# Performance work log

Hardware: AMD Instinct MI355X
Metric: run time of the kernel (lower is better)

Reference implementation:

```python
import jax, jax.numpy as jnp
import numpy as np

BATCH, SEQ, D_MODEL = 2, 4096, 1024
D_STATE, EXPAND = 64, 2
D_INNER = D_MODEL * EXPAND


def setup_inputs() -> dict:
    key = jax.random.key(0)
    ks = jax.random.split(key, 12)
    s = 0.02
    return {
        "x": jax.random.normal(ks[0], (BATCH, SEQ, D_MODEL), dtype=jnp.float32),
        "W_in": jax.random.normal(ks[1], (D_MODEL, 2 * D_INNER), dtype=jnp.float32) * s,
        "b_in": jnp.zeros((2 * D_INNER,), dtype=jnp.float32),
        "W_xp": jax.random.normal(ks[2], (D_INNER, D_STATE), dtype=jnp.float32) * s,
        "b_xp": jnp.zeros((D_STATE,), dtype=jnp.float32),
        "W_dt": jax.random.normal(ks[3], (D_INNER, D_MODEL), dtype=jnp.float32) * s,
        "b_dt": jnp.zeros((D_MODEL,), dtype=jnp.float32),
        "W_out": jax.random.normal(ks[4], (D_INNER, D_MODEL), dtype=jnp.float32) * s,
        "b_out": jnp.zeros((D_MODEL,), dtype=jnp.float32),
        "A_log": jax.random.normal(ks[5], (D_STATE,), dtype=jnp.float32),
        "D": jax.random.normal(ks[6], (D_MODEL,), dtype=jnp.float32),
    }


def _silu(v):
    return v * jax.nn.sigmoid(v)


def reference(x, W_in, b_in, W_xp, b_xp, W_dt, b_dt, W_out, b_out, A_log, D):
    # in_proj -> split into inner stream and residual gate
    xr = x @ W_in + b_in                       # [B,S,2*d_inner]
    x_inner, res = jnp.split(xr, 2, axis=-1)   # each [B,S,d_inner]
    x_inner = _silu(x_inner)

    A = -jnp.exp(A_log)                        # [N]
    delta = jax.nn.softplus(x_inner @ W_dt + b_dt)  # [B,S,d_model]
    mean_delta = delta.mean(axis=-1)           # [B,S] (scalar dt per step, as in source)
    a = jnp.exp(A[None, None, :] * mean_delta[..., None])  # [B,S,N] discrete A
    bx = x_inner @ W_xp + b_xp                 # [B,S,N] input injection

    # sequential selective-scan recurrence: state = a_t * state + bx_t
    def step(state, inp):
        a_t, bx_t = inp                        # [B,N] each
        state = a_t * state + bx_t
        return state, state.sum(axis=-1)       # emit per-batch scalar

    init = jnp.zeros((x.shape[0], D_STATE), dtype=x.dtype)
    _, s_sum = jax.lax.scan(step, init, (a.transpose(1, 0, 2), bx.transpose(1, 0, 2)))
    s_sum = s_sum.T                            # [B,S]

    y = s_sum[..., None] * x_inner             # [B,S,d_inner]
    y = y * _silu(res)
    out = y @ W_out + b_out + x * D
    return out
```

## Files before the change

### kernel.cpp

```cpp
#include <hip/hip_runtime.h>

#define SEQ 4096
#define DMODEL 1024
#define DSTATE 64
#define DINNER 2048
#define MROWS 8192
#define NCAT 1152
#define NCHUNK 64
#define LCHUNK 64

typedef __attribute__((ext_vector_type(8))) __bf16 bf16x8;
typedef __attribute__((ext_vector_type(8))) short short8;
typedef __attribute__((ext_vector_type(4))) float floatx4;

__device__ inline float bf2f(short s) {
  union { unsigned u; float f; } c;
  c.u = ((unsigned)(unsigned short)s) << 16;
  return c.f;
}
__device__ inline short f2bf(float f) {
  union { float f; unsigned u; } c; c.f = f;
  unsigned r = 0x7fffu + ((c.u >> 16) & 1u);
  return (short)((c.u + r) >> 16);
}
__device__ inline float silu_f(float v) {
  return v * __builtin_amdgcn_rcpf(1.f + __expf(-v));
}
__device__ inline float softplus_f(float v) {
  return fmaxf(v, 0.f) + log1pf(__expf(-fabsf(v)));
}
__device__ inline void gld_lds16(const void* g, void* l) {
  __builtin_amdgcn_global_load_lds(
      (__attribute__((address_space(1))) void*)g,
      (__attribute__((address_space(3))) void*)l, 16, 0, 0);
}

__device__ inline size_t permOff(int r, int k, int K) {
  return (((size_t)(r >> 4) * (K >> 3) + (k >> 3)) << 7) + ((r & 15) << 3) + (k & 7);
}

#define PP0 4096
#define PP1 (PP0 + 4096)
#define PP2 (PP1 + 2048)
#define PP3 (PP2 + 128)
#define PP4 (PP3 + 2048)

__device__ void tile_transpose_perm(const float* __restrict__ in, short* __restrict__ out,
                                    int R, int C, int bx, int by, float (*tile)[33]) {
  const int tx = threadIdx.x & 31, ty = threadIdx.x >> 5;
  const int cb = bx * 32, rb = by * 32;
#pragma unroll
  for (int i = 0; i < 32; i += 8) {
    int r = rb + ty + i, c = cb + tx;
    tile[ty + i][tx] = (r < R && c < C) ? in[(size_t)r * C + c] : 0.f;
  }
  __syncthreads();
#pragma unroll
  for (int i = 0; i < 32; i += 8) {
    int orow = cb + ty + i, oc = rb + tx;
    if (orow < C && oc < R) out[permOff(orow, oc, R)] = f2bf(tile[tx][ty + i]);
  }
}

__global__ void prepass_kernel(const float* __restrict__ x, short* __restrict__ x_bf,
                               const float* __restrict__ W_in, short* __restrict__ Wt_in,
                               const float* __restrict__ W_dt, const float* __restrict__ W_xp,
                               short* __restrict__ Bcat,
                               const float* __restrict__ W_out, short* __restrict__ Wt_out) {
  __shared__ float tile[32][33];
  const int blk = blockIdx.x;
  if (blk < PP0) {
    int o = blk * 256 + threadIdx.x;
    int m = o & 15, rest = o >> 4;
    int c = rest & 127, p = rest >> 7;
    const float* src = x + ((size_t)(p * 16 + m)) * 1024 + c * 8;
    float4 v0 = ((const float4*)src)[0];
    float4 v1 = ((const float4*)src)[1];
    short8 ov;
    ov[0] = f2bf(v0.x); ov[1] = f2bf(v0.y); ov[2] = f2bf(v0.z); ov[3] = f2bf(v0.w);
    ov[4] = f2bf(v1.x); ov[5] = f2bf(v1.y); ov[6] = f2bf(v1.z); ov[7] = f2bf(v1.w);
    ((short8*)x_bf)[o] = ov;
  } else if (blk < PP1) {
    int t = blk - PP0;
    tile_transpose_perm(W_in, Wt_in, 1024, 4096, t & 127, t >> 7, tile);
  } else if (blk < PP2) {
    int t = blk - PP1;
    tile_transpose_perm(W_dt, Bcat, 2048, 1024, t & 31, t >> 5, tile);
  } else if (blk < PP3) {
    int t = blk - PP2;
    tile_transpose_perm(W_xp, Bcat + (size_t)1024 * DINNER, 2048, 64, t & 1, t >> 1, tile);
  } else {
    int t = blk - PP3;
    tile_transpose_perm(W_out, Wt_out, 2048, 1024, t & 31, t >> 5, tile);
  }
}

template <int MODE, int KTOT, int KSL, int NB, int Z>
__global__ __launch_bounds__(256) void gemm_bt(
    const short* __restrict__ A, const short* __restrict__ Bt,
    const float* __restrict__ bias,
    void* __restrict__ out0, void* __restrict__ out1)
{
  __shared__ __attribute__((aligned(16))) short sA[128 * 64];
  __shared__ __attribute__((aligned(16))) short sB[128 * 64];

  const int tid = threadIdx.x;
  const int lane = tid & 63;
  const int w = tid >> 6;
  const int wr = w >> 1, wc = w & 1;
  const int m = lane & 15, quad = lane >> 4;

  const int xcd = blockIdx.x & 7;
  const int rest = blockIdx.x >> 3;
  constexpr int PXB = 8 * NB;
  const int z = rest / PXB;
  const int q2 = rest - z * PXB;
  const int bM = (xcd * 8 + (q2 & 7)) * 128;
  const int bN = (q2 >> 3) * 128;
  constexpr int N = NB * 128;

  floatx4 acc[4][4] = {};

  const size_t PS = (size_t)KTOT * 16;
  const short* Apan0 = A  + ((size_t)(bM >> 4) + w) * PS + lane * 8;
  const short* Apan1 = Apan0 + 4 * PS;
  const short* Bpan0 = Bt + ((size_t)(bN >> 4) + w) * PS + lane * 8;
  const short* Bpan1 = Bpan0 + 4 * PS;
  short* dA0 = sA + w * 1024;
  short* dA1 = sA + (w + 4) * 1024;
  short* dB0 = sB + w * 1024;
  short* dB1 = sB + (w + 4) * 1024;

  const int kbeg = z * KSL;
  for (int k0 = kbeg; k0 < kbeg + KSL; k0 += 64) {
    __syncthreads();
    const size_t ko = (size_t)k0 * 16;
    gld_lds16(Apan0 + ko,       dA0);
    gld_lds16(Apan0 + ko + 512, dA0 + 512);
    gld_lds16(Apan1 + ko,       dA1);
    gld_lds16(Apan1 + ko + 512, dA1 + 512);
    gld_lds16(Bpan0 + ko,       dB0);
    gld_lds16(Bpan0 + ko + 512, dB0 + 512);
    gld_lds16(Bpan1 + ko,       dB1);
    gld_lds16(Bpan1 + ko + 512, dB1 + 512);
    __syncthreads();
#pragma unroll
    for (int kh = 0; kh < 2; ++kh) {
      bf16x8 af[4], bf[4];
#pragma unroll
      for (int rt = 0; rt < 4; ++rt)
        af[rt] = *(const bf16x8*)(sA + (wr * 4 + rt) * 1024 + (kh * 4 + quad) * 128 + m * 8);
#pragma unroll
      for (int ct = 0; ct < 4; ++ct)
        bf[ct] = *(const bf16x8*)(sB + (wc * 4 + ct) * 1024 + (kh * 4 + quad) * 128 + m * 8);
#pragma unroll
      for (int rt = 0; rt < 4; ++rt)
#pragma unroll
        for (int ct = 0; ct < 4; ++ct)
          acc[rt][ct] = __builtin_amdgcn_mfma_f32_16x16x32_bf16(af[rt], bf[ct], acc[rt][ct], 0, 0, 0);
    }
  }

  const int rowbase = bM + wr * 64;
  const int colbase = bN + wc * 64;

  if (MODE == 0) {
    short* dst = (bN < DINNER) ? (short*)out0 : (short*)out1;
    const int cb = (bN < DINNER) ? colbase : colbase - DINNER;
#pragma unroll
    for (int rt = 0; rt < 4; ++rt) {
      const size_t rowPan = ((size_t)((rowbase >> 4) + rt)) << 8;
#pragma unroll
      for (int ct = 0; ct < 4; ++ct) {
        const int colA = colbase + ct * 16 + m;
        const int colP = cb + ct * 16 + m;
        const size_t base = ((rowPan + (colP >> 3)) << 7) + (colP & 7) + ((size_t)quad * 32);
#pragma unroll
        for (int reg = 0; reg < 4; ++reg) {
          float val = acc[rt][ct][reg] + bias[colA];
          dst[base + reg * 8] = f2bf(silu_f(val));
        }
      }
    }
  } else {
    if (NB == 9 && colbase >= 1088) return;
    short* dst = (short*)out0 + (size_t)z * MROWS * N;
#pragma unroll
    for (int rt = 0; rt < 4; ++rt)
#pragma unroll
      for (int ct = 0; ct < 4; ++ct) {
        const int col = colbase + ct * 16 + m;
#pragma unroll
        for (int reg = 0; reg < 4; ++reg) {
          const int r = rowbase + rt * 16 + quad * 4 + reg;
          dst[(size_t)r * N + col] = f2bf(acc[rt][ct][reg]);
        }
      }
  }
}

template <int MODE, int KTOT, int KSL, int NT, int ZS>
__global__ __launch_bounds__(512, 2) void gemm256(
    const short* __restrict__ A, const short* __restrict__ Bt,
    const float* __restrict__ bias,
    void* __restrict__ out0, void* __restrict__ out1)
{
  __shared__ __attribute__((aligned(16))) short sA[4 * 8192];
  __shared__ __attribute__((aligned(16))) short sB[4 * 8192];

  const int tid = threadIdx.x;
  const int lane = tid & 63;
  const int w = tid >> 6;
  const int wr = w >> 2, wc = w & 3;
  const int m = lane & 15, quad = lane >> 4;

  const int xcd = blockIdx.x & 7;
  const int q = blockIdx.x >> 3;
  const int mt = xcd * 4 + (q & 3);
  const int rest = q >> 2;
  const int ntile = rest % NT;
  const int z = rest / NT;
  const int bM = mt * 256, bN = ntile * 256;
  const int kbeg = z * KSL;

  floatx4 acc[8][4] = {};

  const size_t PS = (size_t)KTOT * 16;
  const short* Ag0 = A  + ((size_t)(bM >> 4) + w) * PS + (size_t)kbeg * 16 + lane * 8;
  const short* Ag1 = Ag0 + 8 * PS;
  const short* Bg0 = Bt + ((size_t)(bN >> 4) + w) * PS + (size_t)kbeg * 16 + lane * 8;
  const short* Bg1 = Bg0 + 8 * PS;

  constexpr int NTILES = KSL / 32;

  auto STAGE = [&](int t, int slot) {
    const size_t go = (size_t)t << 9;
    short* da = sA + slot * 8192 + w * 512;
    short* db = sB + slot * 8192 + w * 512;
    gld_lds16(Ag0 + go, da);
    gld_lds16(Ag1 + go, da + 4096);
    gld_lds16(Bg0 + go, db);
    gld_lds16(Bg1 + go, db + 4096);
  };
  auto COMPUTE = [&](int slot) {
    const short* sa = sA + slot * 8192 + wr * 4096 + quad * 128 + m * 8;
    const short* sb = sB + slot * 8192 + wc * 2048 + quad * 128 + m * 8;
    bf16x8 af[8], bf[4];
#pragma unroll
    for (int rt = 0; rt < 8; ++rt) af[rt] = *(const bf16x8*)(sa + rt * 512);
#pragma unroll
    for (int ct = 0; ct < 4; ++ct) bf[ct] = *(const bf16x8*)(sb + ct * 512);
#pragma unroll
    for (int rt = 0; rt < 8; ++rt)
#pragma unroll
      for (int ct = 0; ct < 4; ++ct)
        acc[rt][ct] = __builtin_amdgcn_mfma_f32_16x16x32_bf16(af[rt], bf[ct], acc[rt][ct], 0, 0, 0);
  };

  STAGE(0, 0); STAGE(1, 1); STAGE(2, 2);
  asm volatile("s_waitcnt vmcnt(8)" ::: "memory");
  __builtin_amdgcn_s_barrier();

#pragma unroll 1
  for (int t = 0; t < NTILES - 3; ++t) {
    STAGE(t + 3, (t + 3) & 3);
    COMPUTE(t & 3);
    asm volatile("s_waitcnt vmcnt(8)" ::: "memory");
    __builtin_amdgcn_s_barrier();
  }
  COMPUTE((NTILES - 3) & 3);
  asm volatile("s_waitcnt vmcnt(4)" ::: "memory");
  __builtin_amdgcn_s_barrier();
  COMPUTE((NTILES - 2) & 3);
  asm volatile("s_waitcnt vmcnt(0)" ::: "memory");
  __builtin_amdgcn_s_barrier();
  COMPUTE((NTILES - 1) & 3);

  const int rowbase = bM + wr * 128;
  const int colbase = bN + wc * 64;

  if constexpr (MODE == 0) {
    short* dst = (bN < DINNER) ? (short*)out0 : (short*)out1;
    const int cb = (bN < DINNER) ? colbase : colbase - DINNER;
#pragma unroll
    for (int rt = 0; rt < 8; ++rt) {
      const size_t rowPan = ((size_t)(rowbase >> 4) + rt) << 8;
#pragma unroll
      for (int ct = 0; ct < 4; ++ct) {
        const int colA = colbase + ct * 16 + m;
        const int colP = cb + ct * 16 + m;
        const size_t base = ((rowPan + (colP >> 3)) << 7) + (colP & 7) + ((size_t)quad * 32);
        const float bv = bias[colA];
#pragma unroll
        for (int reg = 0; reg < 4; ++reg) {
          float val = acc[rt][ct][reg] + bv;
          dst[base + reg * 8] = f2bf(silu_f(val));
        }
      }
    }
  } else {
    constexpr int N = NT * 256;
    short* dst = (short*)out0 + (size_t)z * MROWS * N;
#pragma unroll
    for (int rt = 0; rt < 8; ++rt)
#pragma unroll
      for (int ct = 0; ct < 4; ++ct) {
        const int col = colbase + ct * 16 + m;
#pragma unroll
        for (int reg = 0; reg < 4; ++reg) {
          const int r = rowbase + rt * 16 + quad * 4 + reg;
          dst[(size_t)r * N + col] = f2bf(acc[rt][ct][reg]);
        }
      }
  }
}

__global__ void g2_epilogue(const short* __restrict__ p, const float* __restrict__ b_dt,
                            const float* __restrict__ b_xp,
                            float* __restrict__ md_sum, float* __restrict__ bx) {
  const int row = blockIdx.x * 4 + (threadIdx.x >> 6);
  const int lane = threadIdx.x & 63;
  const size_t base0 = (size_t)row * NCAT;
  const size_t base1 = base0 + (size_t)MROWS * NCAT;
  short8 a0 = *(const short8*)(p + base0 + lane * 16);
  short8 a1 = *(const short8*)(p + base0 + lane * 16 + 8);
  short8 c0 = *(const short8*)(p + base1 + lane * 16);
  short8 c1 = *(const short8*)(p + base1 + lane * 16 + 8);
  float s = 0.f;
#pragma unroll
  for (int j = 0; j < 8; ++j) {
    s += softplus_f(bf2f(a0[j]) + bf2f(c0[j]) + b_dt[lane * 16 + j]);
    s += softplus_f(bf2f(a1[j]) + bf2f(c1[j]) + b_dt[lane * 16 + 8 + j]);
  }
  s += __shfl_xor(s, 1);  s += __shfl_xor(s, 2);  s += __shfl_xor(s, 4);
  s += __shfl_xor(s, 8);  s += __shfl_xor(s, 16); s += __shfl_xor(s, 32);
  if (lane == 0) md_sum[row] = s;
  bx[(size_t)row * DSTATE + lane] =
      bf2f(p[base0 + 1024 + lane]) + bf2f(p[base1 + 1024 + lane]) + b_xp[lane];
}

__global__ void g4_epilogue(const short* __restrict__ p, const float* __restrict__ b_out,
                            const float* __restrict__ x, const float* __restrict__ Dv,
                            float* __restrict__ out) {
  const int r = blockIdx.x, c = threadIdx.x * 4;
  const size_t o = (size_t)r * DMODEL + c;
  short4 a0 = *(const short4*)(p + o);
  short4 a1 = *(const short4*)(p + (size_t)MROWS * DMODEL + o);
  float4 xv = *(const float4*)(x + o);
  float4 ov;
  ov.x = bf2f(a0.x) + bf2f(a1.x) + b_out[c + 0] + xv.x * Dv[c + 0];
  ov.y = bf2f(a0.y) + bf2f(a1.y) + b_out[c + 1] + xv.y * Dv[c + 1];
  ov.z = bf2f(a0.z) + bf2f(a1.z) + b_out[c + 2] + xv.z * Dv[c + 2];
  ov.w = bf2f(a0.w) + bf2f(a1.w) + b_out[c + 3] + xv.w * Dv[c + 3];
  *(float4*)(out + o) = ov;
}

__global__ void scan_phase1(const float* __restrict__ md_sum, const float* __restrict__ A_log,
                            const float* __restrict__ bx,
                            float* __restrict__ chunk_prod, float* __restrict__ chunk_end) {
  const int n = threadIdx.x;
  const int c = blockIdx.x & (NCHUNK - 1);
  const int b = blockIdx.x >> 6;
  const float An = -__expf(A_log[n]);
  float prod = 1.f, st = 0.f;
  const int t0 = c * LCHUNK;
#pragma unroll 4
  for (int i = 0; i < LCHUNK; ++i) {
    const int t = t0 + i;
    const float md = md_sum[b * SEQ + t] * (1.f / DMODEL);
    const float a = __expf(An * md);
    st = a * st + bx[((size_t)(b * SEQ + t)) * DSTATE + n];
    prod *= a;
  }
  chunk_prod[(b * NCHUNK + c) * DSTATE + n] = prod;
  chunk_end [(b * NCHUNK + c) * DSTATE + n] = st;
}

__global__ void scan_phase3(const float* __restrict__ md_sum, const float* __restrict__ A_log,
                            const float* __restrict__ bx,
                            const float* __restrict__ chunk_prod,
                            const float* __restrict__ chunk_end,
                            float* __restrict__ s_sum) {
  const int n = threadIdx.x;
  const int c = blockIdx.x & (NCHUNK - 1);
  const int b = blockIdx.x >> 6;
  const float An = -__expf(A_log[n]);
  float st = 0.f;
  for (int cc = 0; cc < c; ++cc) {
    const size_t idx = ((size_t)(b * NCHUNK + cc)) * DSTATE + n;
    st = chunk_prod[idx] * st + chunk_end[idx];
  }
  const int t0 = c * LCHUNK;
#pragma unroll 4
  for (int i = 0; i < LCHUNK; ++i) {
    const int t = t0 + i;
    const float md = md_sum[b * SEQ + t] * (1.f / DMODEL);
    const float a = __expf(An * md);
    st = a * st + bx[((size_t)(b * SEQ + t)) * DSTATE + n];
    float v = st;
    v += __shfl_xor(v, 32); v += __shfl_xor(v, 16); v += __shfl_xor(v, 8);
    v += __shfl_xor(v, 4);  v += __shfl_xor(v, 2);  v += __shfl_xor(v, 1);
    if (n == 0) s_sum[b * SEQ + t] = v;
  }
}

__global__ void ymul_kernel(const short* __restrict__ xi, const short* __restrict__ g,
                            const float* __restrict__ s_sum, short* __restrict__ y) {
  const int o = blockIdx.x * 256 + threadIdx.x;
  const int row = ((o >> 12) << 4) | (o & 15);
  const size_t base = (size_t)o * 8;
  const float s = s_sum[row];
  short8 xv = *(const short8*)(xi + base);
  short8 gv = *(const short8*)(g + base);
  short8 yv;
#pragma unroll
  for (int k = 0; k < 8; ++k) yv[k] = f2bf(s * bf2f(xv[k]) * bf2f(gv[k]));
  *(short8*)(y + base) = yv;
}

extern "C" void kernel_launch(void* const* d_in, const int* in_sizes, int n_in,
                              void* d_out, int out_size, void* d_ws, size_t ws_size,
                              hipStream_t stream) {
  const float* x     = (const float*)d_in[0];
  const float* W_in  = (const float*)d_in[1];
  const float* b_in  = (const float*)d_in[2];
  const float* W_xp  = (const float*)d_in[3];
  const float* b_xp  = (const float*)d_in[4];
  const float* W_dt  = (const float*)d_in[5];
  const float* b_dt  = (const float*)d_in[6];
  const float* W_out = (const float*)d_in[7];
  const float* b_out = (const float*)d_in[8];
  const float* A_log = (const float*)d_in[9];
  const float* Dv    = (const float*)d_in[10];

  char* ws = (char*)d_ws;
  size_t off = 0;
  auto alloc = [&](size_t bytes) -> void* {
    void* p = (void*)(ws + off);
    off += (bytes + 255) & ~(size_t)255;
    return p;
  };
  short* x_bf    = (short*)alloc((size_t)MROWS * DMODEL * 2);
  short* Wt_in   = (short*)alloc((size_t)4096 * 1024 * 2);
  short* Bcat    = (short*)alloc((size_t)NCAT * DINNER * 2);
  short* Wt_out  = (short*)alloc((size_t)1024 * 2048 * 2);
  short* xi      = (short*)alloc((size_t)MROWS * DINNER * 2);
  short* gbuf    = (short*)alloc((size_t)MROWS * DINNER * 2);
  short* ybuf    = (short*)alloc((size_t)MROWS * DINNER * 2);
  short* p2      = (short*)alloc((size_t)2 * MROWS * NCAT * 2);
  float* md_sum  = (float*)alloc((size_t)MROWS * 4);
  float* bx      = (float*)alloc((size_t)MROWS * DSTATE * 4);
  float* cprod   = (float*)alloc((size_t)2 * NCHUNK * DSTATE * 4);
  float* cend    = (float*)alloc((size_t)2 * NCHUNK * DSTATE * 4);
  float* s_sum   = (float*)alloc((size_t)MROWS * 4);

  prepass_kernel<<<PP4, 256, 0, stream>>>(x, x_bf, W_in, Wt_in, W_dt, W_xp, Bcat, W_out, Wt_out);

  gemm256<0, 1024, 1024, 16, 1><<<512, 512, 0, stream>>>(x_bf, Wt_in, b_in, xi, gbuf);
  gemm_bt<1, 2048, 1024, 9, 2><<<1152, 256, 0, stream>>>(xi, Bcat, nullptr, p2, nullptr);
  g2_epilogue<<<MROWS / 4, 256, 0, stream>>>(p2, b_dt, b_xp, md_sum, bx);
  scan_phase1<<<2 * NCHUNK, DSTATE, 0, stream>>>(md_sum, A_log, bx, cprod, cend);
  scan_phase3<<<2 * NCHUNK, DSTATE, 0, stream>>>(md_sum, A_log, bx, cprod, cend, s_sum);
  ymul_kernel<<<MROWS * DINNER / 8 / 256, 256, 0, stream>>>(xi, gbuf, s_sum, ybuf);
  gemm256<1, 2048, 1024, 4, 2><<<256, 512, 0, stream>>>(ybuf, Wt_out, nullptr, xi, nullptr);
  g4_epilogue<<<MROWS, 256, 0, stream>>>(xi, b_out, x, Dv, (float*)d_out);
}
```

Measured before the change: 423.1 us.

## Split GEMM main loop into two half-phases with interleaved staging and priority

Restructures the GEMM main loop into two phases per K-tile. Each phase loads half the A fragments, issues half of the next tile's global-to-LDS staging (A, then B), barriers, and runs 16 MFMAs at raised wave priority. The aim is to interleave memory issue with matrix math and cut register pressure by holding only four A fragments at a time. In exchange it adds an extra barrier per tile and handles the epilogue tiles with conditional waitcnt values inside the loop.

After: 388.5 us. 8.2% less time.

```diff
diff --git a/kernel.cpp b/kernel.cpp
--- a/kernel.cpp
+++ b/kernel.cpp
@@ -233,48 +233,67 @@
 
   constexpr int NTILES = KSL / 32;
 
-  auto STAGE = [&](int t, int slot) {
+  auto STAGE_A = [&](int t) {
     const size_t go = (size_t)t << 9;
-    short* da = sA + slot * 8192 + w * 512;
-    short* db = sB + slot * 8192 + w * 512;
+    short* da = sA + ((t & 3) << 13) + w * 512;
     gld_lds16(Ag0 + go, da);
     gld_lds16(Ag1 + go, da + 4096);
+  };
+  auto STAGE_B = [&](int t) {
+    const size_t go = (size_t)t << 9;
+    short* db = sB + ((t & 3) << 13) + w * 512;
     gld_lds16(Bg0 + go, db);
     gld_lds16(Bg1 + go, db + 4096);
   };
-  auto COMPUTE = [&](int slot) {
-    const short* sa = sA + slot * 8192 + wr * 4096 + quad * 128 + m * 8;
-    const short* sb = sB + slot * 8192 + wc * 2048 + quad * 128 + m * 8;
-    bf16x8 af[8], bf[4];
-#pragma unroll
-    for (int rt = 0; rt < 8; ++rt) af[rt] = *(const bf16x8*)(sa + rt * 512);
-#pragma unroll
-    for (int ct = 0; ct < 4; ++ct) bf[ct] = *(const bf16x8*)(sb + ct * 512);
-#pragma unroll
-    for (int rt = 0; rt < 8; ++rt)
-#pragma unroll
-      for (int ct = 0; ct < 4; ++ct)
-        acc[rt][ct] = __builtin_amdgcn_mfma_f32_16x16x32_bf16(af[rt], bf[ct], acc[rt][ct], 0, 0, 0);
-  };
-
-  STAGE(0, 0); STAGE(1, 1); STAGE(2, 2);
+
+  STAGE_A(0); STAGE_B(0); STAGE_A(1); STAGE_B(1); STAGE_A(2); STAGE_B(2);
   asm volatile("s_waitcnt vmcnt(8)" ::: "memory");
   __builtin_amdgcn_s_barrier();
 
 #pragma unroll 1
-  for (int t = 0; t < NTILES - 3; ++t) {
-    STAGE(t + 3, (t + 3) & 3);
-    COMPUTE(t & 3);
-    asm volatile("s_waitcnt vmcnt(8)" ::: "memory");
+  for (int t = 0; t < NTILES; ++t) {
+    const short* sa = sA + ((t & 3) << 13) + wr * 4096 + quad * 128 + m * 8;
+    const short* sb = sB + ((t & 3) << 13) + wc * 2048 + quad * 128 + m * 8;
+    bf16x8 af0[4], af1[4], bf[4];
+
+#pragma unroll
+    for (int rt = 0; rt < 4; ++rt) af0[rt] = *(const bf16x8*)(sa + rt * 512);
+#pragma unroll
+    for (int ct = 0; ct < 4; ++ct) bf[ct] = *(const bf16x8*)(sb + ct * 512);
+    if (t < NTILES - 3) STAGE_A(t + 3);
+    __builtin_amdgcn_sched_barrier(0);
     __builtin_amdgcn_s_barrier();
-  }
-  COMPUTE((NTILES - 3) & 3);
-  asm volatile("s_waitcnt vmcnt(4)" ::: "memory");
-  __builtin_amdgcn_s_barrier();
-  COMPUTE((NTILES - 2) & 3);
-  asm volatile("s_waitcnt vmcnt(0)" ::: "memory");
-  __builtin_amdgcn_s_barrier();
-  COMPUTE((NTILES - 1) & 3);
+    __builtin_amdgcn_sched_barrier(0);
+    __builtin_amdgcn_s_setprio(1);
+#pragma unroll
+    for (int rt = 0; rt < 4; ++rt)
+#pragma unroll
+      for (int ct = 0; ct < 4; ++ct)
+        acc[rt][ct] = __builtin_amdgcn_mfma_f32_16x16x32_bf16(af0[rt], bf[ct], acc[rt][ct], 0, 0, 0);
+    __builtin_amdgcn_s_setprio(0);
+    __builtin_amdgcn_sched_barrier(0);
+    __builtin_amdgcn_s_barrier();
+
+#pragma unroll
+    for (int rt = 0; rt < 4; ++rt) af1[rt] = *(const bf16x8*)(sa + (4 + rt) * 512);
+    if (t < NTILES - 3) STAGE_B(t + 3);
+    __builtin_amdgcn_sched_barrier(0);
+    __builtin_amdgcn_s_barrier();
+    __builtin_amdgcn_sched_barrier(0);
+    __builtin_amdgcn_s_setprio(1);
+#pragma unroll
+    for (int rt = 0; rt < 4; ++rt)
+#pragma unroll
+      for (int ct = 0; ct < 4; ++ct)
+        acc[4 + rt][ct] = __builtin_amdgcn_mfma_f32_16x16x32_bf16(af1[rt], bf[ct], acc[4 + rt][ct], 0, 0, 0);
+    __builtin_amdgcn_s_setprio(0);
+    __builtin_amdgcn_sched_barrier(0);
+
+    if (t < NTILES - 3)       asm volatile("s_waitcnt vmcnt(8)" ::: "memory");
+    else if (t == NTILES - 3) asm volatile("s_waitcnt vmcnt(4)" ::: "memory");
+    else if (t == NTILES - 2) asm volatile("s_waitcnt vmcnt(0)" ::: "memory");
+    if (t < NTILES - 1) __builtin_amdgcn_s_barrier();
+  }
 
   const int rowbase = bM + wr * 128;
   const int colbase = bN + wc * 64;
```
